# Optimization experiments

Hardware: AMD Instinct MI355X
Metric: run time of the kernel (lower is better)

Reference implementation:

```python
import jax, jax.numpy as jnp
import numpy as np

N = 100000   # num_nodes
E = 1250000  # num_edges
D = 64       # embedding_dim
L = 3        # num_layers


def setup_inputs() -> dict:
    key = jax.random.key(0)
    k1, k2, k3, k4 = jax.random.split(key, 4)
    edge_index = jax.random.randint(k1, (2, E), 0, N, dtype=jnp.int64)
    edge_label_index = jax.random.randint(k2, (2, E), 0, N, dtype=jnp.int64)
    # xavier_uniform init of Embedding(N, D)
    bound = float(np.sqrt(6.0 / (N + D)))
    emb_weight = jax.random.uniform(k3, (N, D), jnp.float32, -bound, bound)
    alpha = jnp.full((L + 1,), 1.0 / (L + 1), dtype=jnp.float32)
    return {"edge_index": edge_index, "edge_label_index": edge_label_index,
            "emb_weight": emb_weight, "alpha": alpha}


def reference(edge_index, edge_label_index, emb_weight, alpha):
    src, dst = edge_index[0], edge_index[1]
    n = emb_weight.shape[0]
    # gcn_norm (LGConv, no self-loops): deg over destination, sym normalization
    deg = jax.ops.segment_sum(jnp.ones(src.shape[0], emb_weight.dtype), dst, num_segments=n)
    dis = jnp.where(deg > 0, jax.lax.rsqrt(jnp.where(deg > 0, deg, 1.0)), 0.0)
    w = dis[src] * dis[dst]  # [E]

    weights = jax.nn.softmax(alpha)  # [L+1]
    x = emb_weight
    out = x * weights[0]
    for i in range(L):
        # LGConv: out[dst] += norm * x[src]
        x = jax.ops.segment_sum(w[:, None] * x[src], dst, num_segments=n)
        out = out + x * weights[i + 1]

    # predict_link_embedding: per-edge dot product
    return (out[edge_label_index[0]] * out[edge_label_index[1]]).sum(axis=-1)
```

## Files before the change

kernel.cpp:

```cpp
#include <hip/hip_runtime.h>
#include <math.h>

#define DIM 64
#define PART_T 4096
#define BK_SHIFT 9
#define BK_SPAN 512

typedef _Float16 half8 __attribute__((ext_vector_type(8)));


__device__ __forceinline__ half8 shfl_xor_h8(half8 v, int mask) {
    int4 iv;
    __builtin_memcpy(&iv, &v, 16);
    iv.x = __shfl_xor(iv.x, mask, 64);
    iv.y = __shfl_xor(iv.y, mask, 64);
    iv.z = __shfl_xor(iv.z, mask, 64);
    iv.w = __shfl_xor(iv.w, mask, 64);
    half8 r;
    __builtin_memcpy(&r, &iv, 16);
    return r;
}

__device__ __forceinline__ half8 dpp_ror8_h8(half8 v) {
    int4 iv;
    __builtin_memcpy(&iv, &v, 16);
    int4 r;
    r.x = __builtin_amdgcn_update_dpp(0, iv.x, 0x128, 0xF, 0xF, true);
    r.y = __builtin_amdgcn_update_dpp(0, iv.y, 0x128, 0xF, 0xF, true);
    r.z = __builtin_amdgcn_update_dpp(0, iv.z, 0x128, 0xF, 0xF, true);
    r.w = __builtin_amdgcn_update_dpp(0, iv.w, 0x128, 0xF, 0xF, true);
    half8 out;
    __builtin_memcpy(&out, &r, 16);
    return out;
}

__device__ __forceinline__ float dpp_sum8_f32(float v) {
    int x = __float_as_int(v);
    v += __int_as_float(__builtin_amdgcn_update_dpp(0, x, 0xB1, 0xF, 0xF, true));
    x = __float_as_int(v);
    v += __int_as_float(__builtin_amdgcn_update_dpp(0, x, 0x4E, 0xF, 0xF, true));
    x = __float_as_int(v);
    v += __int_as_float(__builtin_amdgcn_update_dpp(0, x, 0x141, 0xF, 0xF, true));
    return v;
}


__global__ void count_kernel(const int* __restrict__ dst, int* __restrict__ gcount,
                             int E, int K) {
    __shared__ int h[256];
    int t = threadIdx.x;
    h[t] = 0;
    __syncthreads();
    int tile = blockIdx.x * PART_T;
    int n = E - tile; if (n > PART_T) n = PART_T;
    for (int i = t; i < n; i += 256)
        atomicAdd(&h[dst[tile + i] >> BK_SHIFT], 1);
    __syncthreads();
    if (t < K && h[t] > 0) atomicAdd(&gcount[t], h[t]);
}

__global__ void bscan_kernel(const int* __restrict__ gcount, int* __restrict__ bbase,
                             int* __restrict__ gcursor, int* __restrict__ rowptr,
                             int K, int N, int E) {
    __shared__ int s[256];
    int t = threadIdx.x;
    int v = (t < K) ? gcount[t] : 0;
    s[t] = v;
    __syncthreads();
    #pragma unroll
    for (int off = 1; off < 256; off <<= 1) {
        int add = (t >= off) ? s[t - off] : 0;
        __syncthreads();
        s[t] += add;
        __syncthreads();
    }
    int excl = s[t] - v;
    if (t < K) { bbase[t] = excl; gcursor[t] = excl; }
    if (t == 0) rowptr[N] = E;
}


__global__ void part_kernel(const int* __restrict__ src, const int* __restrict__ dst,
                            int* __restrict__ gcursor, unsigned int* __restrict__ part,
                            int E, int K) {
    __shared__ unsigned int tmp_rec[PART_T];
    __shared__ unsigned int reord[PART_T];
    __shared__ unsigned char tmp_bkt[PART_T];
    __shared__ unsigned char tmp_bkt2[PART_T];
    __shared__ int hist[256];
    __shared__ int scanbuf[256];
    __shared__ int lstart[256];
    __shared__ int cursor[256];
    __shared__ int gbase[256];
    int t = threadIdx.x;
    int tile = blockIdx.x * PART_T;
    int n = E - tile; if (n > PART_T) n = PART_T;

    hist[t] = 0;
    __syncthreads();

    for (int i = t; i < n; i += 256) {
        int s = src[tile + i];
        int d = dst[tile + i];
        int b = d >> BK_SHIFT;
        tmp_rec[i] = (unsigned int)s | ((unsigned int)(d & (BK_SPAN - 1)) << 17);
        tmp_bkt[i] = (unsigned char)b;
        atomicAdd(&hist[b], 1);
    }
    __syncthreads();

    int hv = hist[t];
    scanbuf[t] = hv;
    __syncthreads();
    #pragma unroll
    for (int off = 1; off < 256; off <<= 1) {
        int add = (t >= off) ? scanbuf[t - off] : 0;
        __syncthreads();
        scanbuf[t] += add;
        __syncthreads();
    }
    int excl = scanbuf[t] - hv;
    lstart[t] = excl;
    cursor[t] = excl;
    if (t < K && hv > 0) gbase[t] = atomicAdd(&gcursor[t], hv);
    __syncthreads();

    for (int i = t; i < n; i += 256) {
        int b = tmp_bkt[i];
        int r = atomicAdd(&cursor[b], 1);
        reord[r] = tmp_rec[i];
        tmp_bkt2[r] = (unsigned char)b;
    }
    __syncthreads();

    for (int i = t; i < n; i += 256) {
        int b = tmp_bkt2[i];
        part[gbase[b] + (i - lstart[b])] = reord[i];
    }
}


__global__ void csr_kernel(const unsigned int* __restrict__ part, const int* __restrict__ bbase,
                           const int* __restrict__ gcount, int* __restrict__ rowptr,
                           int* __restrict__ csr_src, float* __restrict__ dis,
                           float* __restrict__ invdis, int N) {
    __shared__ int h[BK_SPAN];
    __shared__ int scanbuf[256];
    int b = blockIdx.x;
    int t = threadIdx.x;
    int base = bbase[b];
    int cnt  = gcount[b];
    int nodeBase = b << BK_SHIFT;

    h[t] = 0; h[t + 256] = 0;
    __syncthreads();

    for (int j = t; j < cnt; j += 256) {
        unsigned int rec = part[base + j];
        atomicAdd(&h[rec >> 17], 1);
    }
    __syncthreads();

    #pragma unroll
    for (int k = 0; k < 2; ++k) {
        int i = t + k * 256;
        int idx = nodeBase + i;
        if (idx < N) {
            int d = h[i];
            float df = (float)d;
            dis[idx]    = d > 0 ? 1.0f / sqrtf(df) : 0.0f;
            invdis[idx] = d > 0 ? sqrtf(df) : 0.0f;
        }
    }

    int a = h[2 * t], c = h[2 * t + 1];
    int pairsum = a + c;
    scanbuf[t] = pairsum;
    __syncthreads();
    #pragma unroll
    for (int off = 1; off < 256; off <<= 1) {
        int add = (t >= off) ? scanbuf[t - off] : 0;
        __syncthreads();
        scanbuf[t] += add;
        __syncthreads();
    }
    int excl = scanbuf[t] - pairsum;
    __syncthreads();
    h[2 * t]     = excl;
    h[2 * t + 1] = excl + a;
    __syncthreads();

    #pragma unroll
    for (int k = 0; k < 2; ++k) {
        int i = t + k * 256;
        int idx = nodeBase + i;
        if (idx < N) rowptr[idx] = base + h[i];
    }
    __syncthreads();

    for (int j = t; j < cnt; j += 256) {
        unsigned int rec = part[base + j];
        int dl = (int)(rec >> 17);
        int s  = (int)(rec & 0x1FFFFu);
        int p = atomicAdd(&h[dl], 1);
        csr_src[base + p] = s;
    }
}


__global__ void conv_kernel(const float* __restrict__ emb, const float* __restrict__ dis,
                            half8* __restrict__ g0, int n8) {
    int i = blockIdx.x * blockDim.x + threadIdx.x;
    if (i >= n8) return;
    int v = i >> 3;
    float d = dis[v];
    const float4* e4 = (const float4*)emb;
    float4 a = e4[2 * i], b = e4[2 * i + 1];
    half8 h;
    h[0] = (_Float16)(d * a.x); h[1] = (_Float16)(d * a.y);
    h[2] = (_Float16)(d * a.z); h[3] = (_Float16)(d * a.w);
    h[4] = (_Float16)(d * b.x); h[5] = (_Float16)(d * b.y);
    h[6] = (_Float16)(d * b.z); h[7] = (_Float16)(d * b.w);
    g0[i] = h;
}


__device__ __forceinline__ void softmax4(const float* __restrict__ alpha, float* w) {
    float a0 = alpha[0], a1 = alpha[1], a2 = alpha[2], a3 = alpha[3];
    float m = fmaxf(fmaxf(a0, a1), fmaxf(a2, a3));
    float e0 = expf(a0 - m), e1 = expf(a1 - m), e2 = expf(a2 - m), e3 = expf(a3 - m);
    float s = 1.0f / (e0 + e1 + e2 + e3);
    w[0] = e0 * s; w[1] = e1 * s; w[2] = e2 * s; w[3] = e3 * s;
}

__global__ void spmm_kernel(const int* __restrict__ rowptr, const int* __restrict__ csr_src,
                            const float* __restrict__ dis,
                            const half8* __restrict__ gin, half8* __restrict__ gout, int N) {
    int lane = threadIdx.x & 63;
    int wave = blockIdx.x * (blockDim.x >> 6) + (threadIdx.x >> 6);
    int v = wave * 2 + (lane >> 5);
    int slot = (lane >> 3) & 3;
    int sub  = lane & 7;
    bool valid = v < N;
    int beg = 0, end = 0;
    if (valid) { beg = rowptr[v]; end = rowptr[v + 1]; }
    half8 acc = (half8)(_Float16)0;
    for (int j = beg + slot; j < end; j += 4) {
        acc = acc + gin[csr_src[j] * 8 + sub];
    }
    acc = acc + dpp_ror8_h8(acc);
    acc = acc + shfl_xor_h8(acc, 16);
    if (valid && (lane & 31) < 8) {
        float d = dis[v];
        float d2 = d * d;
        half8 o;
        #pragma unroll
        for (int k = 0; k < 8; ++k) o[k] = (_Float16)(d2 * (float)acc[k]);
        gout[v * 8 + sub] = o;
    }
}

__global__ void spmm_final_kernel(const int* __restrict__ rowptr, const int* __restrict__ csr_src,
                                  const float* __restrict__ dis, const float* __restrict__ invdis,
                                  const float* __restrict__ emb, const half8* __restrict__ g1,
                                  const half8* __restrict__ g2, half8* __restrict__ out,
                                  const float* __restrict__ alpha, int N) {
    int lane = threadIdx.x & 63;
    int wave = blockIdx.x * (blockDim.x >> 6) + (threadIdx.x >> 6);
    int v = wave * 2 + (lane >> 5);
    int slot = (lane >> 3) & 3;
    int sub  = lane & 7;
    bool valid = v < N;
    int beg = 0, end = 0;
    if (valid) { beg = rowptr[v]; end = rowptr[v + 1]; }
    half8 acc = (half8)(_Float16)0;
    for (int j = beg + slot; j < end; j += 4) {
        acc = acc + g2[csr_src[j] * 8 + sub];
    }
    acc = acc + dpp_ror8_h8(acc);
    acc = acc + shfl_xor_h8(acc, 16);
    if (valid && (lane & 31) < 8) {
        float w[4];
        softmax4(alpha, w);
        float d  = dis[v];
        float iv = invdis[v];
        const float4* e4 = (const float4*)emb;
        float4 ea = e4[v * 16 + sub * 2];
        float4 eb = e4[v * 16 + sub * 2 + 1];
        half8 h1 = g1[v * 8 + sub];
        half8 h2 = g2[v * 8 + sub];
        float ef[8] = {ea.x, ea.y, ea.z, ea.w, eb.x, eb.y, eb.z, eb.w};
        half8 o;
        #pragma unroll
        for (int k = 0; k < 8; ++k) {
            float x1 = (float)h1[k] * iv;
            float x2 = (float)h2[k] * iv;
            float x3 = d * (float)acc[k];
            float val = w[0] * ef[k] + w[1] * x1 + w[2] * x2 + w[3] * x3;
            o[k] = (_Float16)val;
        }
        out[v * 8 + sub] = o;
    }
}

__global__ void dot_kernel(const int* __restrict__ a, const int* __restrict__ b,
                           const half8* __restrict__ out, float* __restrict__ res, int E) {
    long long g = (long long)blockIdx.x * blockDim.x + threadIdx.x;
    int e   = (int)(g >> 3);
    int sub = (int)(g & 7);
    if (e >= E) return;
    int ia = a[e];
    int ib = b[e];
    half8 va = out[ia * 8 + sub];
    half8 vb = out[ib * 8 + sub];
#if __has_builtin(__builtin_amdgcn_fdot2)
    float v = 0.f;
    v = __builtin_amdgcn_fdot2(__builtin_shufflevector(va, va, 0, 1),
                               __builtin_shufflevector(vb, vb, 0, 1), v, false);
    v = __builtin_amdgcn_fdot2(__builtin_shufflevector(va, va, 2, 3),
                               __builtin_shufflevector(vb, vb, 2, 3), v, false);
    v = __builtin_amdgcn_fdot2(__builtin_shufflevector(va, va, 4, 5),
                               __builtin_shufflevector(vb, vb, 4, 5), v, false);
    v = __builtin_amdgcn_fdot2(__builtin_shufflevector(va, va, 6, 7),
                               __builtin_shufflevector(vb, vb, 6, 7), v, false);
#else
    float v = 0.f;
    #pragma unroll
    for (int k = 0; k < 8; ++k) v += (float)va[k] * (float)vb[k];
#endif
    v = dpp_sum8_f32(v);
    if (sub == 0) res[e] = v;
}


static inline size_t align256(size_t x) { return (x + 255) & ~(size_t)255; }

extern "C" void kernel_launch(void* const* d_in, const int* in_sizes, int n_in,
                              void* d_out, int out_size, void* d_ws, size_t ws_size,
                              hipStream_t stream) {
    const int* edge_index = (const int*)d_in[0];
    const int* edge_label = (const int*)d_in[1];
    const float* emb      = (const float*)d_in[2];
    const float* alpha    = (const float*)d_in[3];

    const int E = in_sizes[0] / 2;
    const int N = in_sizes[2] / DIM;
    const int K = (N + BK_SPAN - 1) >> BK_SHIFT;

    const int* src = edge_index;
    const int* dst = edge_index + E;
    const int* la  = edge_label;
    const int* lb  = edge_label + E;

    char* ws = (char*)d_ws;
    size_t off = 0;
    float* dis     = (float*)(ws + off); off = align256(off + (size_t)N * 4);
    float* invdis  = (float*)(ws + off); off = align256(off + (size_t)N * 4);
    int*   rowptr  = (int*)(ws + off);   off = align256(off + (size_t)(N + 1) * 4);
    int*   gcount  = (int*)(ws + off);   off = align256(off + (size_t)256 * 4);
    int*   bbase   = (int*)(ws + off);   off = align256(off + (size_t)256 * 4);
    int*   gcursor = (int*)(ws + off);   off = align256(off + (size_t)256 * 4);
    unsigned int* part = (unsigned int*)(ws + off); off = align256(off + (size_t)E * 4);
    int*   csr_src = (int*)(ws + off);   off = align256(off + (size_t)E * 4);
    half8* g0      = (half8*)(ws + off); off = align256(off + (size_t)N * DIM * 2);
    half8* g1      = (half8*)(ws + off); off = align256(off + (size_t)N * DIM * 2);
    half8* g2      = (half8*)(ws + off); off = align256(off + (size_t)N * DIM * 2);
    half8* outbuf  = (half8*)(ws + off); off = align256(off + (size_t)N * DIM * 2);
    (void)ws_size;

    const int B = 256;
    const int gridT = (E + PART_T - 1) / PART_T;

    hipMemsetAsync(gcount, 0, 256 * 4, stream);
    count_kernel<<<gridT, B, 0, stream>>>(dst, gcount, E, K);
    bscan_kernel<<<1, B, 0, stream>>>(gcount, bbase, gcursor, rowptr, K, N, E);

    part_kernel<<<gridT, B, 0, stream>>>(src, dst, gcursor, part, E, K);

    csr_kernel<<<K, B, 0, stream>>>(part, bbase, gcount, rowptr, csr_src, dis, invdis, N);

    const int n8 = N * DIM / 8;
    conv_kernel<<<(n8 + B - 1) / B, B, 0, stream>>>(emb, dis, g0, n8);

    const int nodesPerBlock = (B / 64) * 2;
    const int gridS = (N + nodesPerBlock - 1) / nodesPerBlock;
    spmm_kernel<<<gridS, B, 0, stream>>>(rowptr, csr_src, dis, g0, g1, N);
    spmm_kernel<<<gridS, B, 0, stream>>>(rowptr, csr_src, dis, g1, g2, N);
    spmm_final_kernel<<<gridS, B, 0, stream>>>(rowptr, csr_src, dis, invdis, emb, g1, g2,
                                               outbuf, alpha, N);

    const long long dthreads = (long long)E * 8;
    const int gridD = (int)((dthreads + B - 1) / B);
    dot_kernel<<<gridD, B, 0, stream>>>(la, lb, outbuf, (float*)d_out, E);
}
```

Measured before the change: 265.8 us.

## Pad CSR rows to multiples of four for vectorized int4 index loads

Each node's neighbor list is padded to a multiple of four entries, with the padding pointing at a zero sentinel row N in each feature buffer. Rows are addressed through separate start/end arrays. The SpMM kernels then load column indices as int4 and accumulate into two independent half8 registers, which cuts index load instructions and adds memory-level parallelism. In exchange there is extra padded gather traffic to the sentinel row and a larger csr buffer, and invdis is dropped in favour of computing 1/d on the fly.

```diff
diff --git a/kernel.cpp b/kernel.cpp
--- a/kernel.cpp
+++ b/kernel.cpp
@@ -5,6 +5,7 @@
 #define PART_T 4096
 #define BK_SHIFT 9
 #define BK_SPAN 512
+#define BK_PAD 2048
 
 typedef _Float16 half8 __attribute__((ext_vector_type(8)));
 
@@ -60,8 +61,7 @@
 }
 
 __global__ void bscan_kernel(const int* __restrict__ gcount, int* __restrict__ bbase,
-                             int* __restrict__ gcursor, int* __restrict__ rowptr,
-                             int K, int N, int E) {
+                             int* __restrict__ gcursor, int K) {
     __shared__ int s[256];
     int t = threadIdx.x;
     int v = (t < K) ? gcount[t] : 0;
@@ -76,7 +76,6 @@
     }
     int excl = s[t] - v;
     if (t < K) { bbase[t] = excl; gcursor[t] = excl; }
-    if (t == 0) rowptr[N] = E;
 }
 
 
@@ -141,15 +140,17 @@
 
 
 __global__ void csr_kernel(const unsigned int* __restrict__ part, const int* __restrict__ bbase,
-                           const int* __restrict__ gcount, int* __restrict__ rowptr,
-                           int* __restrict__ csr_src, float* __restrict__ dis,
-                           float* __restrict__ invdis, int N) {
+                           const int* __restrict__ gcount, int* __restrict__ pstart,
+                           int* __restrict__ pend, int* __restrict__ csr_src,
+                           float* __restrict__ dis, int N) {
     __shared__ int h[BK_SPAN];
+    __shared__ int pfx[BK_SPAN + 1];
     __shared__ int scanbuf[256];
     int b = blockIdx.x;
     int t = threadIdx.x;
     int base = bbase[b];
     int cnt  = gcount[b];
+    int qbase = ((base + 3) & ~3) + b * BK_PAD;
     int nodeBase = b << BK_SHIFT;
 
     h[t] = 0; h[t + 256] = 0;
@@ -159,6 +160,33 @@
         unsigned int rec = part[base + j];
         atomicAdd(&h[rec >> 17], 1);
     }
+    __syncthreads();
+
+    int d0 = h[2 * t], d1 = h[2 * t + 1];
+    {
+        int i0 = nodeBase + 2 * t, i1 = i0 + 1;
+        if (i0 < N) dis[i0] = d0 > 0 ? 1.0f / sqrtf((float)d0) : 0.0f;
+        if (i1 < N) dis[i1] = d1 > 0 ? 1.0f / sqrtf((float)d1) : 0.0f;
+    }
+    int p0 = (d0 + 3) & ~3;
+    int p1 = (d1 + 3) & ~3;
+    int pairsum = p0 + p1;
+    scanbuf[t] = pairsum;
+    __syncthreads();
+    #pragma unroll
+    for (int off = 1; off < 256; off <<= 1) {
+        int add = (t >= off) ? scanbuf[t - off] : 0;
+        __syncthreads();
+        scanbuf[t] += add;
+        __syncthreads();
+    }
+    int excl = scanbuf[t] - pairsum;
+    __syncthreads();
+    pfx[2 * t]     = excl;
+    pfx[2 * t + 1] = excl + p0;
+    h[2 * t]       = excl;
+    h[2 * t + 1]   = excl + p0;
+    if (t == 255) pfx[BK_SPAN] = scanbuf[255];
     __syncthreads();
 
     #pragma unroll
@@ -166,35 +194,9 @@
         int i = t + k * 256;
         int idx = nodeBase + i;
         if (idx < N) {
-            int d = h[i];
-            float df = (float)d;
-            dis[idx]    = d > 0 ? 1.0f / sqrtf(df) : 0.0f;
-            invdis[idx] = d > 0 ? sqrtf(df) : 0.0f;
+            pstart[idx] = qbase + pfx[i];
+            pend[idx]   = qbase + pfx[i + 1];
         }
-    }
-
-    int a = h[2 * t], c = h[2 * t + 1];
-    int pairsum = a + c;
-    scanbuf[t] = pairsum;
-    __syncthreads();
-    #pragma unroll
-    for (int off = 1; off < 256; off <<= 1) {
-        int add = (t >= off) ? scanbuf[t - off] : 0;
-        __syncthreads();
-        scanbuf[t] += add;
-        __syncthreads();
-    }
-    int excl = scanbuf[t] - pairsum;
-    __syncthreads();
-    h[2 * t]     = excl;
-    h[2 * t + 1] = excl + a;
-    __syncthreads();
-
-    #pragma unroll
-    for (int k = 0; k < 2; ++k) {
-        int i = t + k * 256;
-        int idx = nodeBase + i;
-        if (idx < N) rowptr[idx] = base + h[i];
     }
     __syncthreads();
 
@@ -203,14 +205,29 @@
         int dl = (int)(rec >> 17);
         int s  = (int)(rec & 0x1FFFFu);
         int p = atomicAdd(&h[dl], 1);
-        csr_src[base + p] = s;
+        csr_src[qbase + p] = s;
+    }
+    __syncthreads();
+
+    #pragma unroll
+    for (int k = 0; k < 2; ++k) {
+        int i = t + k * 256;
+        int endp = pfx[i + 1];
+        for (int p = h[i]; p < endp; ++p) csr_src[qbase + p] = N;
     }
 }
 
 
 __global__ void conv_kernel(const float* __restrict__ emb, const float* __restrict__ dis,
-                            half8* __restrict__ g0, int n8) {
+                            half8* __restrict__ g0, half8* __restrict__ g1,
+                            half8* __restrict__ g2, int n8, int N) {
     int i = blockIdx.x * blockDim.x + threadIdx.x;
+    if (i < 8) {
+        half8 z = (half8)(_Float16)0;
+        g0[N * 8 + i] = z;
+        g1[N * 8 + i] = z;
+        g2[N * 8 + i] = z;
+    }
     if (i >= n8) return;
     int v = i >> 3;
     float d = dis[v];
@@ -233,8 +250,8 @@
     w[0] = e0 * s; w[1] = e1 * s; w[2] = e2 * s; w[3] = e3 * s;
 }
 
-__global__ void spmm_kernel(const int* __restrict__ rowptr, const int* __restrict__ csr_src,
-                            const float* __restrict__ dis,
+__global__ void spmm_kernel(const int* __restrict__ pstart, const int* __restrict__ pend,
+                            const int* __restrict__ csr_src, const float* __restrict__ dis,
                             const half8* __restrict__ gin, half8* __restrict__ gout, int N) {
     int lane = threadIdx.x & 63;
     int wave = blockIdx.x * (blockDim.x >> 6) + (threadIdx.x >> 6);
@@ -243,11 +260,18 @@
     int sub  = lane & 7;
     bool valid = v < N;
     int beg = 0, end = 0;
-    if (valid) { beg = rowptr[v]; end = rowptr[v + 1]; }
-    half8 acc = (half8)(_Float16)0;
-    for (int j = beg + slot; j < end; j += 4) {
-        acc = acc + gin[csr_src[j] * 8 + sub];
-    }
+    if (valid) { beg = pstart[v]; end = pend[v]; }
+    const int4* csr4 = (const int4*)csr_src;
+    half8 acc0 = (half8)(_Float16)0;
+    half8 acc1 = (half8)(_Float16)0;
+    for (int j = beg + slot * 4; j < end; j += 16) {
+        int4 c = csr4[j >> 2];
+        acc0 = acc0 + gin[c.x * 8 + sub];
+        acc1 = acc1 + gin[c.y * 8 + sub];
+        acc0 = acc0 + gin[c.z * 8 + sub];
+        acc1 = acc1 + gin[c.w * 8 + sub];
+    }
+    half8 acc = acc0 + acc1;
     acc = acc + dpp_ror8_h8(acc);
     acc = acc + shfl_xor_h8(acc, 16);
     if (valid && (lane & 31) < 8) {
@@ -260,8 +284,8 @@
     }
 }
 
-__global__ void spmm_final_kernel(const int* __restrict__ rowptr, const int* __restrict__ csr_src,
-                                  const float* __restrict__ dis, const float* __restrict__ invdis,
+__global__ void spmm_final_kernel(const int* __restrict__ pstart, const int* __restrict__ pend,
+                                  const int* __restrict__ csr_src, const float* __restrict__ dis,
                                   const float* __restrict__ emb, const half8* __restrict__ g1,
                                   const half8* __restrict__ g2, half8* __restrict__ out,
                                   const float* __restrict__ alpha, int N) {
@@ -272,18 +296,25 @@
     int sub  = lane & 7;
     bool valid = v < N;
     int beg = 0, end = 0;
-    if (valid) { beg = rowptr[v]; end = rowptr[v + 1]; }
-    half8 acc = (half8)(_Float16)0;
-    for (int j = beg + slot; j < end; j += 4) {
-        acc = acc + g2[csr_src[j] * 8 + sub];
-    }
+    if (valid) { beg = pstart[v]; end = pend[v]; }
+    const int4* csr4 = (const int4*)csr_src;
+    half8 acc0 = (half8)(_Float16)0;
+    half8 acc1 = (half8)(_Float16)0;
+    for (int j = beg + slot * 4; j < end; j += 16) {
+        int4 c = csr4[j >> 2];
+        acc0 = acc0 + g2[c.x * 8 + sub];
+        acc1 = acc1 + g2[c.y * 8 + sub];
+        acc0 = acc0 + g2[c.z * 8 + sub];
+        acc1 = acc1 + g2[c.w * 8 + sub];
+    }
+    half8 acc = acc0 + acc1;
     acc = acc + dpp_ror8_h8(acc);
     acc = acc + shfl_xor_h8(acc, 16);
     if (valid && (lane & 31) < 8) {
         float w[4];
         softmax4(alpha, w);
         float d  = dis[v];
-        float iv = invdis[v];
+        float iv = d > 0.0f ? 1.0f / d : 0.0f;
         const float4* e4 = (const float4*)emb;
         float4 ea = e4[v * 16 + sub * 2];
         float4 eb = e4[v * 16 + sub * 2 + 1];
@@ -355,16 +386,16 @@
     char* ws = (char*)d_ws;
     size_t off = 0;
     float* dis     = (float*)(ws + off); off = align256(off + (size_t)N * 4);
-    float* invdis  = (float*)(ws + off); off = align256(off + (size_t)N * 4);
-    int*   rowptr  = (int*)(ws + off);   off = align256(off + (size_t)(N + 1) * 4);
+    int*   pstart  = (int*)(ws + off);   off = align256(off + (size_t)N * 4);
+    int*   pend    = (int*)(ws + off);   off = align256(off + (size_t)N * 4);
     int*   gcount  = (int*)(ws + off);   off = align256(off + (size_t)256 * 4);
     int*   bbase   = (int*)(ws + off);   off = align256(off + (size_t)256 * 4);
     int*   gcursor = (int*)(ws + off);   off = align256(off + (size_t)256 * 4);
     unsigned int* part = (unsigned int*)(ws + off); off = align256(off + (size_t)E * 4);
-    int*   csr_src = (int*)(ws + off);   off = align256(off + (size_t)E * 4);
-    half8* g0      = (half8*)(ws + off); off = align256(off + (size_t)N * DIM * 2);
-    half8* g1      = (half8*)(ws + off); off = align256(off + (size_t)N * DIM * 2);
-    half8* g2      = (half8*)(ws + off); off = align256(off + (size_t)N * DIM * 2);
+    int*   csr_src = (int*)(ws + off);   off = align256(off + ((size_t)E + (size_t)K * BK_PAD + 64) * 4);
+    half8* g0      = (half8*)(ws + off); off = align256(off + (size_t)(N + 1) * DIM * 2);
+    half8* g1      = (half8*)(ws + off); off = align256(off + (size_t)(N + 1) * DIM * 2);
+    half8* g2      = (half8*)(ws + off); off = align256(off + (size_t)(N + 1) * DIM * 2);
     half8* outbuf  = (half8*)(ws + off); off = align256(off + (size_t)N * DIM * 2);
     (void)ws_size;
 
@@ -373,20 +404,20 @@
 
     hipMemsetAsync(gcount, 0, 256 * 4, stream);
     count_kernel<<<gridT, B, 0, stream>>>(dst, gcount, E, K);
-    bscan_kernel<<<1, B, 0, stream>>>(gcount, bbase, gcursor, rowptr, K, N, E);
+    bscan_kernel<<<1, B, 0, stream>>>(gcount, bbase, gcursor, K);
 
     part_kernel<<<gridT, B, 0, stream>>>(src, dst, gcursor, part, E, K);
 
-    csr_kernel<<<K, B, 0, stream>>>(part, bbase, gcount, rowptr, csr_src, dis, invdis, N);
+    csr_kernel<<<K, B, 0, stream>>>(part, bbase, gcount, pstart, pend, csr_src, dis, N);
 
     const int n8 = N * DIM / 8;
-    conv_kernel<<<(n8 + B - 1) / B, B, 0, stream>>>(emb, dis, g0, n8);
+    conv_kernel<<<(n8 + B - 1) / B, B, 0, stream>>>(emb, dis, g0, g1, g2, n8, N);
 
     const int nodesPerBlock = (B / 64) * 2;
     const int gridS = (N + nodesPerBlock - 1) / nodesPerBlock;
-    spmm_kernel<<<gridS, B, 0, stream>>>(rowptr, csr_src, dis, g0, g1, N);
-    spmm_kernel<<<gridS, B, 0, stream>>>(rowptr, csr_src, dis, g1, g2, N);
-    spmm_final_kernel<<<gridS, B, 0, stream>>>(rowptr, csr_src, dis, invdis, emb, g1, g2,
+    spmm_kernel<<<gridS, B, 0, stream>>>(pstart, pend, csr_src, dis, g0, g1, N);
+    spmm_kernel<<<gridS, B, 0, stream>>>(pstart, pend, csr_src, dis, g1, g2, N);
+    spmm_final_kernel<<<gridS, B, 0, stream>>>(pstart, pend, csr_src, dis, emb, g1, g2,
                                                outbuf, alpha, N);
 
     const long long dthreads = (long long)E * 8;
```

After: 247.5 us. 6.9% less time.
